# Performance work log

Measured on AMD Instinct MI355X. Metric: run time of the kernel, lower is better.

Reference implementation:

```python
import jax, jax.numpy as jnp
import numpy as np

S, B, D_MODEL, H = 2048, 2, 1024, 16
DH = D_MODEL // H
SCALE = 1.0 / np.sqrt(DH)
NEG_INF = jnp.float32(-1e30)


def setup_inputs() -> dict:
    key = jax.random.key(0)
    ks = jax.random.split(key, 12)
    std = 1.0 / np.sqrt(D_MODEL)
    inp = {
        "query": jax.random.normal(ks[0], (S, B, D_MODEL), jnp.float32),
        "key": jax.random.normal(ks[1], (S, B, D_MODEL), jnp.float32),
        "value": jax.random.normal(ks[2], (S, B, D_MODEL), jnp.float32),
        # causal mask, shape (seq_q, seq_k, 1) per prepare_mask asserts
        "mask": jnp.tril(jnp.ones((S, S), dtype=bool))[:, :, None],
        # params stored (in, out) for x @ W
        "Wq": jax.random.normal(ks[3], (D_MODEL, H * DH), jnp.float32) * std,
        "bq": jnp.zeros((H * DH,), jnp.float32),
        "Wk": jax.random.normal(ks[4], (D_MODEL, H * DH), jnp.float32) * std,
        "bk": jnp.zeros((H * DH,), jnp.float32),
        "Wv": jax.random.normal(ks[5], (D_MODEL, H * DH), jnp.float32) * std,
        "bv": jnp.zeros((H * DH,), jnp.float32),
        "Wo": jax.random.normal(ks[6], (D_MODEL, D_MODEL), jnp.float32) * std,
        "bo": jnp.zeros((D_MODEL,), jnp.float32),
    }
    return inp


def reference(query, key, value, mask, Wq, bq, Wk, bk, Wv, bv, Wo, bo):
    seq_len, batch, _ = query.shape
    # project and split heads: (S, B, H, DH)
    q = (query @ Wq + bq).reshape(seq_len, batch, H, DH)
    k = (key @ Wk + bk).reshape(key.shape[0], batch, H, DH)
    v = (value @ Wv + bv).reshape(value.shape[0], batch, H, DH)
    # scores: (seq_q, batch, heads, seq_k)
    scores = jnp.einsum("ibhd,jbhd->ibhj", q, k) * SCALE
    # mask (seq_q, seq_k, batch_or_1) -> broadcast to (seq_q, batch, 1, seq_k)
    m = jnp.transpose(mask, (0, 2, 1))[:, :, None, :]
    scores = jnp.where(m, scores, NEG_INF)
    attn = jax.nn.softmax(scores, axis=-1)  # dropout_prob=0.0 (eval)
    x = jnp.einsum("ibhj,jbhd->ibhd", attn, v)
    x = x.reshape(seq_len, batch, H * DH)
    return x @ Wo + bo
```

## Files before the change

### kernel.cpp

```cpp
#include <hip/hip_runtime.h>
#include <hip/hip_bf16.h>
#include <cstdint>

#define S_LEN 2048
#define BATCH 2
#define DM    1024
#define NH    16
#define DH    64
#define SL2E  0.18033688011112042f

typedef short s8v __attribute__((ext_vector_type(8)));
typedef float f4v __attribute__((ext_vector_type(4)));

__device__ __forceinline__ ushort f2bf(float x) {
  union { float f; uint32_t u; } v; v.f = x;
  uint32_t r = v.u + 0x7fffu + ((v.u >> 16) & 1u);
  return (ushort)(r >> 16);
}
__device__ __forceinline__ uint32_t fbits(float x) {
  union { float f; uint32_t u; } v; v.f = x; return v.u;
}
__device__ __forceinline__ uint32_t bfrnd(uint32_t u) {
  return u + 0x7fffu + ((u >> 16) & 1u);
}
__device__ __forceinline__ uint32_t packbf(uint32_t flo, uint32_t fhi) {
  return __builtin_amdgcn_perm(bfrnd(fhi), bfrnd(flo), 0x07060302u);
}

typedef __attribute__((address_space(1))) const void gas_void;
typedef __attribute__((address_space(3))) void las_void;
__device__ __forceinline__ void gld16(void* l, const void* g) {
  __builtin_amdgcn_global_load_lds((gas_void*)(uintptr_t)g,
                                   (las_void*)(uintptr_t)l, 16, 0, 0);
}

__global__ __launch_bounds__(256)
void wtrans(const float* W0, const float* W1, const float* W2, const float* W3,
            ushort* T0, ushort* T1, ushort* T2, ushort* T3) {
  const float* W; ushort* T;
  switch (blockIdx.z) {
    case 0:  W = W0; T = T0; break;
    case 1:  W = W1; T = T1; break;
    case 2:  W = W2; T = T2; break;
    default: W = W3; T = T3; break;
  }
  __shared__ ushort tile[32][33];
  const int n0 = blockIdx.x * 32, k0 = blockIdx.y * 32;
  const int tx = threadIdx.x, ty = threadIdx.y;
  #pragma unroll
  for (int r = ty; r < 32; r += 8)
    tile[r][tx] = f2bf(W[(size_t)(k0 + r) * DM + n0 + tx]);
  __syncthreads();
  #pragma unroll
  for (int r = ty; r < 32; r += 8)
    T[(size_t)(n0 + r) * DM + k0 + tx] = tile[tx][r];
}

__global__ __launch_bounds__(256)
void castx(const float* __restrict__ X0, const float* __restrict__ X1,
           const float* __restrict__ X2,
           ushort* __restrict__ O0, ushort* __restrict__ O1,
           ushort* __restrict__ O2) {
  const float* X; ushort* O;
  switch (blockIdx.y) {
    case 0:  X = X0; O = O0; break;
    case 1:  X = X1; O = O1; break;
    default: X = X2; O = O2; break;
  }
  const size_t i = ((size_t)blockIdx.x * 256 + threadIdx.x) * 4;
  const float4 v = *(const float4*)(X + i);
  ushort4 h;
  h.x = f2bf(v.x); h.y = f2bf(v.y); h.z = f2bf(v.z); h.w = f2bf(v.w);
  *(ushort4*)(O + i) = h;
}

__global__ __launch_bounds__(256)
void gemm_qkv(const ushort* __restrict__ Xq, const ushort* __restrict__ Xk,
              const ushort* __restrict__ Xv,
              const ushort* __restrict__ Wqt, const ushort* __restrict__ Wkt,
              const ushort* __restrict__ Wvt,
              const float* __restrict__ bq, const float* __restrict__ bk,
              const float* __restrict__ bv,
              ushort* __restrict__ Qh, ushort* __restrict__ Kh,
              ushort* __restrict__ Vt) {
  const int z = blockIdx.z;
  const ushort* A    = z == 0 ? Xq  : z == 1 ? Xk  : Xv;
  const ushort* Bt   = z == 0 ? Wqt : z == 1 ? Wkt : Wvt;
  const float*  bias = z == 0 ? bq  : z == 1 ? bk  : bv;

  __shared__ __align__(16) ushort lds[20480];
  ushort* ldsA = lds;
  ushort* ldsB = lds + 8192;

  const int tid = threadIdx.x, lane = tid & 63, w = tid >> 6;
  const int wr = w >> 1, wc = w & 1;
  const int lrow = lane & 15, quad = lane >> 4;
  const int m0 = blockIdx.x * 128, n0 = blockIdx.y * 128;

  const int srow = lane >> 3;
  const int scol = ((lane & 7) ^ srow) * 8;

  const ushort* gA[4]; ushort* lA[4];
  const ushort* gB[4]; ushort* lB[4];
  #pragma unroll
  for (int t = 0; t < 4; t++) {
    const int c = 4 * w + t;
    gA[t] = A  + (size_t)(m0 + c * 8 + srow) * DM + scol;
    lA[t] = &ldsA[c * 512];
    gB[t] = Bt + (size_t)(n0 + c * 8 + srow) * DM + scol;
    lB[t] = &ldsB[c * 512];
  }

  const int f8 = lrow & 7;
  const ushort *pa[2][4], *pb[2][4];
  #pragma unroll
  for (int kk = 0; kk < 2; kk++)
    #pragma unroll
    for (int i = 0; i < 4; i++) {
      pa[kk][i] = &ldsA[(wr * 64 + i * 16 + lrow) * 64 + (((kk * 4 + quad) ^ f8) * 8)];
      pb[kk][i] = &ldsB[(wc * 64 + i * 16 + lrow) * 64 + (((kk * 4 + quad) ^ f8) * 8)];
    }

  f4v acc[4][4];
  #pragma unroll
  for (int i = 0; i < 4; i++)
    #pragma unroll
    for (int j = 0; j < 4; j++)
      acc[i][j] = f4v{0.f, 0.f, 0.f, 0.f};

  for (int k0 = 0; k0 < DM; k0 += 64) {
    __syncthreads();
    #pragma unroll
    for (int t = 0; t < 4; t++) { gld16(lA[t], gA[t] + k0); gld16(lB[t], gB[t] + k0); }
    __syncthreads();
    #pragma unroll
    for (int kk = 0; kk < 2; kk++) {
      s8v af[4], bf[4];
      #pragma unroll
      for (int i = 0; i < 4; i++) af[i] = *(const s8v*)pa[kk][i];
      #pragma unroll
      for (int j = 0; j < 4; j++) bf[j] = *(const s8v*)pb[kk][j];
      #pragma unroll
      for (int i = 0; i < 4; i++)
        #pragma unroll
        for (int j = 0; j < 4; j++)
          acc[i][j] = __builtin_amdgcn_mfma_f32_16x16x32_bf16(af[i], bf[j], acc[i][j], 0, 0, 0);
    }
  }

  if (z <= 1) {
    ushort* O = (z == 0) ? Qh : Kh;
    #pragma unroll
    for (int i = 0; i < 4; i++)
      #pragma unroll
      for (int j = 0; j < 4; j++) {
        const int n = n0 + wc * 64 + j * 16 + lrow;
        const float bval = bias[n];
        const int mb = m0 + wr * 64 + i * 16 + quad * 4;
        #pragma unroll
        for (int r = 0; r < 4; r++) {
          const int m = mb + r;
          const int s = m >> 1, b = m & 1;
          const int h = n >> 6, d = n & 63;
          O[((size_t)(b * NH + h) * S_LEN + s) * DH + d] = f2bf(acc[i][j][r] + bval);
        }
      }
  } else {
    __syncthreads();
    ushort* tw = lds + w * 5120;
    #pragma unroll
    for (int i = 0; i < 4; i++)
      #pragma unroll
      for (int j = 0; j < 4; j++) {
        const int n_l = j * 16 + lrow;
        const float bval = bias[n0 + wc * 64 + n_l];
        const int sbase = i * 8 + quad * 2;
        const uint32_t p0 = packbf(fbits(acc[i][j][0] + bval), fbits(acc[i][j][2] + bval));
        const uint32_t p1 = packbf(fbits(acc[i][j][1] + bval), fbits(acc[i][j][3] + bval));
        *(uint32_t*)&tw[n_l * 40 + sbase]        = p0;
        *(uint32_t*)&tw[2560 + n_l * 40 + sbase] = p1;
      }
    const int s0 = (m0 >> 1) + wr * 32;
    #pragma unroll
    for (int b = 0; b < 2; b++)
      #pragma unroll
      for (int p = 0; p < 4; p++) {
        const int d_l = p * 16 + (lane >> 2);
        const int c   = lane & 3;
        const s8v v = *(const s8v*)&tw[b * 2560 + d_l * 40 + c * 8];
        const int n = n0 + wc * 64 + d_l;
        const int h = n >> 6, d = n & 63;
        *(s8v*)&Vt[((size_t)(b * NH + h) * DH + d) * S_LEN + s0 + c * 8] = v;
      }
  }
}

__global__ __launch_bounds__(256)
void attn(const ushort* __restrict__ Qh, const ushort* __restrict__ Kh,
          const ushort* __restrict__ Vt, ushort* __restrict__ X,
          float* __restrict__ Opart, float* __restrict__ lpart) {
  __shared__ __align__(16) ushort Klds[2 * 64 * 64];
  __shared__ __align__(16) ushort Vlds[2 * 64 * 64];
  __shared__ __align__(16) ushort Plds[4 * 32 * 72];

  const int tid = threadIdx.x, lane = tid & 63, w = tid >> 6;
  const int lrow = lane & 15, quad = lane >> 4;
  const int bh = blockIdx.x;
  const int slot = blockIdx.y;
  int qt, jlo, jhi, part;
  if (slot < 8) { qt = slot; jlo = 0; jhi = 2 * qt + 2; part = -1; }
  else {
    const int s2 = slot - 8;
    qt = 8 + (s2 >> 1);
    const int half = s2 & 1;
    jlo = half * (qt + 1);
    jhi = jlo + (qt + 1);
    part = s2;
  }
  const int iw = qt * 128 + w * 32;

  const int srow = lane >> 3;
  const int scol = ((lane & 7) ^ srow) * 8;
  const ushort* gK0 = Kh + ((size_t)bh * S_LEN + 2 * w * 8 + srow) * DH + scol;
  const ushort* gK1 = gK0 + 8 * DH;
  const ushort* gV0 = Vt + ((size_t)bh * DH + 2 * w * 8 + srow) * S_LEN + scol;
  const ushort* gV1 = gV0 + 8 * S_LEN;
  ushort* lK0 = &Klds[2 * w * 512]; ushort* lK1 = lK0 + 512;
  ushort* lV0 = &Vlds[2 * w * 512]; ushort* lV1 = lV0 + 512;

  s8v aq[2][2];
  #pragma unroll
  for (int is = 0; is < 2; is++)
    #pragma unroll
    for (int kk = 0; kk < 2; kk++)
      aq[is][kk] = *(const s8v*)(Qh + ((size_t)bh * S_LEN + iw + is * 16 + lrow) * DH +
                                 kk * 32 + quad * 8);

  const int f8 = lrow & 7;
  const ushort* pk[4][2]; const ushort* pv[4][2]; const ushort* pp[2][2];
  #pragma unroll
  for (int s4 = 0; s4 < 4; s4++)
    #pragma unroll
    for (int kk = 0; kk < 2; kk++) {
      pk[s4][kk] = &Klds[(s4 * 16 + lrow) * 64 + (((kk * 4 + quad) ^ f8) * 8)];
      pv[s4][kk] = &Vlds[(s4 * 16 + lrow) * 64 + (((kk * 4 + quad) ^ f8) * 8)];
    }
  #pragma unroll
  for (int is = 0; is < 2; is++)
    #pragma unroll
    for (int kk = 0; kk < 2; kk++)
      pp[is][kk] = &Plds[(w * 32 + is * 16 + lrow) * 72 + kk * 32 + quad * 8];
  ushort* pw = &Plds[w * 32 * 72];

  f4v o[2][4];
  float ls[2][4];
  #pragma unroll
  for (int is = 0; is < 2; is++) {
    #pragma unroll
    for (int d4 = 0; d4 < 4; d4++) o[is][d4] = f4v{0.f, 0.f, 0.f, 0.f};
    #pragma unroll
    for (int r = 0; r < 4; r++) ls[is][r] = 0.f;
  }

  {
    const int b0 = (jlo & 1) * 4096;
    const size_t j0 = (size_t)jlo * 64;
    gld16(lK0 + b0, gK0 + j0 * DH);
    gld16(lK1 + b0, gK1 + j0 * DH);
    gld16(lV0 + b0, gV0 + j0);
    gld16(lV1 + b0, gV1 + j0);
  }

  for (int jt = jlo; jt < jhi; jt++) {
    const int j0 = jt * 64;
    __syncthreads();
    const int cur = (jt & 1) * 4096;
    if (jt + 1 < jhi) {
      const int nxt = ((jt + 1) & 1) * 4096;
      const size_t jn = (size_t)(jt + 1) * 64;
      gld16(lK0 + nxt, gK0 + jn * DH);
      gld16(lK1 + nxt, gK1 + jn * DH);
      gld16(lV0 + nxt, gV0 + jn);
      gld16(lV1 + nxt, gV1 + jn);
    }
    if (j0 > iw + 31) continue;

    f4v sc[2][4];
    #pragma unroll
    for (int is = 0; is < 2; is++)
      #pragma unroll
      for (int s4 = 0; s4 < 4; s4++) sc[is][s4] = f4v{0.f, 0.f, 0.f, 0.f};
    #pragma unroll
    for (int s4 = 0; s4 < 4; s4++) {
      const s8v b0 = *(const s8v*)(pk[s4][0] + cur);
      const s8v b1 = *(const s8v*)(pk[s4][1] + cur);
      sc[0][s4] = __builtin_amdgcn_mfma_f32_16x16x32_bf16(aq[0][0], b0, sc[0][s4], 0, 0, 0);
      sc[1][s4] = __builtin_amdgcn_mfma_f32_16x16x32_bf16(aq[1][0], b0, sc[1][s4], 0, 0, 0);
      sc[0][s4] = __builtin_amdgcn_mfma_f32_16x16x32_bf16(aq[0][1], b1, sc[0][s4], 0, 0, 0);
      sc[1][s4] = __builtin_amdgcn_mfma_f32_16x16x32_bf16(aq[1][1], b1, sc[1][s4], 0, 0, 0);
    }

    const bool needmask = (j0 + 63) > iw;
    #pragma unroll
    for (int is = 0; is < 2; is++)
      #pragma unroll
      for (int s4 = 0; s4 < 4; s4++) {
        const int jg = j0 + s4 * 16 + lrow;
        #pragma unroll
        for (int r = 0; r < 4; r++) {
          float e = exp2f(sc[is][s4][r] * SL2E);
          if (needmask) {
            const int ig = iw + is * 16 + quad * 4 + r;
            e = (jg > ig) ? 0.f : e;
          }
          ls[is][r] += e;
          pw[(is * 16 + quad * 4 + r) * 72 + s4 * 16 + lrow] = f2bf(e);
        }
      }

    s8v ap[2][2];
    #pragma unroll
    for (int is = 0; is < 2; is++)
      #pragma unroll
      for (int kk = 0; kk < 2; kk++) ap[is][kk] = *(const s8v*)pp[is][kk];

    #pragma unroll
    for (int d4 = 0; d4 < 4; d4++) {
      const s8v v0 = *(const s8v*)(pv[d4][0] + cur);
      const s8v v1 = *(const s8v*)(pv[d4][1] + cur);
      o[0][d4] = __builtin_amdgcn_mfma_f32_16x16x32_bf16(ap[0][0], v0, o[0][d4], 0, 0, 0);
      o[1][d4] = __builtin_amdgcn_mfma_f32_16x16x32_bf16(ap[1][0], v0, o[1][d4], 0, 0, 0);
      o[0][d4] = __builtin_amdgcn_mfma_f32_16x16x32_bf16(ap[0][1], v1, o[0][d4], 0, 0, 0);
      o[1][d4] = __builtin_amdgcn_mfma_f32_16x16x32_bf16(ap[1][1], v1, o[1][d4], 0, 0, 0);
    }
  }

  #pragma unroll
  for (int msk = 1; msk < 16; msk <<= 1)
    #pragma unroll
    for (int is = 0; is < 2; is++)
      #pragma unroll
      for (int r = 0; r < 4; r++)
        ls[is][r] += __shfl_xor(ls[is][r], msk, 64);

  if (part < 0) {
    const int bb = bh >> 4, h = bh & 15;
    #pragma unroll
    for (int is = 0; is < 2; is++)
      #pragma unroll
      for (int r = 0; r < 4; r++) {
        const float inv = 1.0f / ls[is][r];
        const int ig = iw + is * 16 + quad * 4 + r;
        #pragma unroll
        for (int d4 = 0; d4 < 4; d4++)
          X[((size_t)ig * BATCH + bb) * DM + h * DH + d4 * 16 + lrow] =
              f2bf(o[is][d4][r] * inv);
      }
  } else {
    float* Op = Opart + ((size_t)(bh * 16 + part)) * 8192 + (size_t)w * 32 * 64;
    #pragma unroll
    for (int is = 0; is < 2; is++)
      #pragma unroll
      for (int r = 0; r < 4; r++) {
        const int row_l = is * 16 + quad * 4 + r;
        #pragma unroll
        for (int d4 = 0; d4 < 4; d4++)
          Op[row_l * 64 + d4 * 16 + lrow] = o[is][d4][r];
      }
    if (lrow == 0) {
      float* lp = lpart + (size_t)(bh * 16 + part) * 128 + w * 32;
      #pragma unroll
      for (int is = 0; is < 2; is++)
        #pragma unroll
        for (int r = 0; r < 4; r++)
          lp[is * 16 + quad * 4 + r] = ls[is][r];
    }
  }
}

__global__ __launch_bounds__(256)
void combine(const float* __restrict__ Opart, const float* __restrict__ lpart,
             ushort* __restrict__ X) {
  const size_t gid = (size_t)blockIdx.x * 256 + threadIdx.x;
  const int dv  = gid & 15;
  const int row = (gid >> 4) & 127;
  const int bh  = (gid >> 11) & 31;
  const int qt8 = gid >> 16;
  const int pa = qt8 * 2, pb = pa + 1;
  const size_t ba = ((size_t)(bh * 16 + pa)) * 8192 + row * 64 + dv * 4;
  const size_t bb_ = ((size_t)(bh * 16 + pb)) * 8192 + row * 64 + dv * 4;
  const float4 va = *(const float4*)(Opart + ba);
  const float4 vb = *(const float4*)(Opart + bb_);
  const float l = lpart[(size_t)(bh * 16 + pa) * 128 + row] +
                  lpart[(size_t)(bh * 16 + pb) * 128 + row];
  const float inv = 1.0f / l;
  const int qpos = (qt8 + 8) * 128 + row;
  const int b = bh >> 4, h = bh & 15;
  ushort4 hv;
  hv.x = f2bf((va.x + vb.x) * inv);
  hv.y = f2bf((va.y + vb.y) * inv);
  hv.z = f2bf((va.z + vb.z) * inv);
  hv.w = f2bf((va.w + vb.w) * inv);
  *(ushort4*)&X[(((size_t)qpos * BATCH + b) * NH + h) * DH + dv * 4] = hv;
}

__global__ __launch_bounds__(256)
void gemm_out(const ushort* __restrict__ A, const ushort* __restrict__ Bt,
              const float* __restrict__ bias, float* __restrict__ C) {
  __shared__ __align__(16) ushort ldsA[128 * 64];
  __shared__ __align__(16) ushort ldsB[128 * 64];

  const int tid = threadIdx.x, lane = tid & 63, w = tid >> 6;
  const int wr = w >> 1, wc = w & 1;
  const int lrow = lane & 15, quad = lane >> 4;
  const int m0 = blockIdx.x * 128, n0 = blockIdx.y * 128;

  const int srow = lane >> 3;
  const int scol = ((lane & 7) ^ srow) * 8;

  const ushort* gA[4]; ushort* lA[4];
  const ushort* gB[4]; ushort* lB[4];
  #pragma unroll
  for (int t = 0; t < 4; t++) {
    const int c = 4 * w + t;
    gA[t] = A  + (size_t)(m0 + c * 8 + srow) * DM + scol;
    lA[t] = &ldsA[c * 512];
    gB[t] = Bt + (size_t)(n0 + c * 8 + srow) * DM + scol;
    lB[t] = &ldsB[c * 512];
  }

  const int f8 = lrow & 7;
  const ushort *pa[2][4], *pb[2][4];
  #pragma unroll
  for (int kk = 0; kk < 2; kk++)
    #pragma unroll
    for (int i = 0; i < 4; i++) {
      pa[kk][i] = &ldsA[(wr * 64 + i * 16 + lrow) * 64 + (((kk * 4 + quad) ^ f8) * 8)];
      pb[kk][i] = &ldsB[(wc * 64 + i * 16 + lrow) * 64 + (((kk * 4 + quad) ^ f8) * 8)];
    }

  f4v acc[4][4];
  #pragma unroll
  for (int i = 0; i < 4; i++)
    #pragma unroll
    for (int j = 0; j < 4; j++)
      acc[i][j] = f4v{0.f, 0.f, 0.f, 0.f};

  for (int k0 = 0; k0 < DM; k0 += 64) {
    __syncthreads();
    #pragma unroll
    for (int t = 0; t < 4; t++) { gld16(lA[t], gA[t] + k0); gld16(lB[t], gB[t] + k0); }
    __syncthreads();
    #pragma unroll
    for (int kk = 0; kk < 2; kk++) {
      s8v af[4], bf[4];
      #pragma unroll
      for (int i = 0; i < 4; i++) af[i] = *(const s8v*)pa[kk][i];
      #pragma unroll
      for (int j = 0; j < 4; j++) bf[j] = *(const s8v*)pb[kk][j];
      #pragma unroll
      for (int i = 0; i < 4; i++)
        #pragma unroll
        for (int j = 0; j < 4; j++)
          acc[i][j] = __builtin_amdgcn_mfma_f32_16x16x32_bf16(af[i], bf[j], acc[i][j], 0, 0, 0);
    }
  }

  #pragma unroll
  for (int i = 0; i < 4; i++)
    #pragma unroll
    for (int j = 0; j < 4; j++) {
      const int n = n0 + wc * 64 + j * 16 + lrow;
      const float bval = bias[n];
      const int mb = m0 + wr * 64 + i * 16 + quad * 4;
      #pragma unroll
      for (int r = 0; r < 4; r++)
        C[(size_t)(mb + r) * DM + n] = acc[i][j][r] + bval;
    }
}

extern "C" void kernel_launch(void* const* d_in, const int* in_sizes, int n_in,
                              void* d_out, int out_size, void* d_ws, size_t ws_size,
                              hipStream_t stream) {
  const float* query = (const float*)d_in[0];
  const float* key_  = (const float*)d_in[1];
  const float* value = (const float*)d_in[2];
  const float* Wq = (const float*)d_in[4];
  const float* bq = (const float*)d_in[5];
  const float* Wk = (const float*)d_in[6];
  const float* bk = (const float*)d_in[7];
  const float* Wv = (const float*)d_in[8];
  const float* bv = (const float*)d_in[9];
  const float* Wo = (const float*)d_in[10];
  const float* bo = (const float*)d_in[11];

  ushort* Wqt = (ushort*)d_ws;
  ushort* Wkt = Wqt + (size_t)1024 * 1024;
  ushort* Wvt = Wkt + (size_t)1024 * 1024;
  ushort* Wot = Wvt + (size_t)1024 * 1024;
  ushort* Xbq = Wot + (size_t)1024 * 1024;
  ushort* Xbk = Xbq + (size_t)4 * 1024 * 1024;
  ushort* Xbv = Xbk + (size_t)4 * 1024 * 1024;
  ushort* Qh  = Xbv + (size_t)4 * 1024 * 1024;
  ushort* Kh  = Qh  + (size_t)4 * 1024 * 1024;
  ushort* Vt  = Kh  + (size_t)4 * 1024 * 1024;
  float*  Opart = (float*)Xbk;
  float*  lpart = (float*)(Vt + (size_t)4 * 1024 * 1024);
  ushort* Xa  = Xbq;

  wtrans<<<dim3(32, 32, 4), dim3(32, 8), 0, stream>>>(Wq, Wk, Wv, Wo,
                                                      Wqt, Wkt, Wvt, Wot);
  castx<<<dim3(4096, 3), 256, 0, stream>>>(query, key_, value, Xbq, Xbk, Xbv);
  gemm_qkv<<<dim3(32, 8, 3), 256, 0, stream>>>(Xbq, Xbk, Xbv,
                                               Wqt, Wkt, Wvt, bq, bk, bv,
                                               Qh, Kh, Vt);
  attn<<<dim3(32, 24), 256, 0, stream>>>(Qh, Kh, Vt, Xa, Opart, lpart);
  combine<<<2048, 256, 0, stream>>>(Opart, lpart, Xa);
  gemm_out<<<dim3(32, 8), 256, 0, stream>>>(Xa, Wot, bo, (float*)d_out);
}
```

Baseline: 262.0 us.

## Give each attention wave its own 32-row task and read K/V from global memory

Attention work is now split per wave instead of per block. Each wave takes one 32-row query strip, with the longest strips split in two and handled longest-first. K and V fragments are loaded straight from global memory into registers, which removes the shared-memory double buffer and the block-wide syncs. The QK MFMA operands are swapped so probabilities are written to LDS as packed 4-element bf16 stores. The weight-transpose and input-cast kernels are also merged into one launch. This trades LDS reuse of K/V across four waves for more global and L2 traffic, in exchange for finer load balancing and fewer syncs.

```diff
diff --git a/kernel.cpp b/kernel.cpp
--- a/kernel.cpp
+++ b/kernel.cpp
@@ -35,43 +35,34 @@
 }
 
 __global__ __launch_bounds__(256)
-void wtrans(const float* W0, const float* W1, const float* W2, const float* W3,
-            ushort* T0, ushort* T1, ushort* T2, ushort* T3) {
-  const float* W; ushort* T;
-  switch (blockIdx.z) {
-    case 0:  W = W0; T = T0; break;
-    case 1:  W = W1; T = T1; break;
-    case 2:  W = W2; T = T2; break;
-    default: W = W3; T = T3; break;
-  }
-  __shared__ ushort tile[32][33];
-  const int n0 = blockIdx.x * 32, k0 = blockIdx.y * 32;
-  const int tx = threadIdx.x, ty = threadIdx.y;
-  #pragma unroll
-  for (int r = ty; r < 32; r += 8)
-    tile[r][tx] = f2bf(W[(size_t)(k0 + r) * DM + n0 + tx]);
-  __syncthreads();
-  #pragma unroll
-  for (int r = ty; r < 32; r += 8)
-    T[(size_t)(n0 + r) * DM + k0 + tx] = tile[tx][r];
-}
-
-__global__ __launch_bounds__(256)
-void castx(const float* __restrict__ X0, const float* __restrict__ X1,
-           const float* __restrict__ X2,
-           ushort* __restrict__ O0, ushort* __restrict__ O1,
-           ushort* __restrict__ O2) {
-  const float* X; ushort* O;
-  switch (blockIdx.y) {
-    case 0:  X = X0; O = O0; break;
-    case 1:  X = X1; O = O1; break;
-    default: X = X2; O = O2; break;
-  }
-  const size_t i = ((size_t)blockIdx.x * 256 + threadIdx.x) * 4;
-  const float4 v = *(const float4*)(X + i);
-  ushort4 h;
-  h.x = f2bf(v.x); h.y = f2bf(v.y); h.z = f2bf(v.z); h.w = f2bf(v.w);
-  *(ushort4*)(O + i) = h;
+void prep(const float* W0, const float* W1, const float* W2, const float* W3,
+          ushort* T0, ushort* T1, ushort* T2, ushort* T3,
+          const float* X0, const float* X1, const float* X2,
+          ushort* O0, ushort* O1, ushort* O2) {
+  const int z = blockIdx.z;
+  if (z < 4) {
+    if (blockIdx.x >= 1024) return;
+    const float* W = z == 0 ? W0 : z == 1 ? W1 : z == 2 ? W2 : W3;
+    ushort*      T = z == 0 ? T0 : z == 1 ? T1 : z == 2 ? T2 : T3;
+    __shared__ ushort tile[32][33];
+    const int n0 = (blockIdx.x & 31) * 32, k0 = (blockIdx.x >> 5) * 32;
+    const int tx = threadIdx.x & 31, ty = threadIdx.x >> 5;
+    #pragma unroll
+    for (int r = ty; r < 32; r += 8)
+      tile[r][tx] = f2bf(W[(size_t)(k0 + r) * DM + n0 + tx]);
+    __syncthreads();
+    #pragma unroll
+    for (int r = ty; r < 32; r += 8)
+      T[(size_t)(n0 + r) * DM + k0 + tx] = tile[tx][r];
+  } else {
+    const float* X = z == 4 ? X0 : z == 5 ? X1 : X2;
+    ushort*      O = z == 4 ? O0 : z == 5 ? O1 : O2;
+    const size_t i = ((size_t)blockIdx.x * 256 + threadIdx.x) * 4;
+    const float4 v = *(const float4*)(X + i);
+    ushort4 h;
+    h.x = f2bf(v.x); h.y = f2bf(v.y); h.z = f2bf(v.z); h.w = f2bf(v.w);
+    *(ushort4*)(O + i) = h;
+  }
 }
 
 __global__ __launch_bounds__(256)
@@ -199,34 +190,31 @@
 void attn(const ushort* __restrict__ Qh, const ushort* __restrict__ Kh,
           const ushort* __restrict__ Vt, ushort* __restrict__ X,
           float* __restrict__ Opart, float* __restrict__ lpart) {
-  __shared__ __align__(16) ushort Klds[2 * 64 * 64];
-  __shared__ __align__(16) ushort Vlds[2 * 64 * 64];
-  __shared__ __align__(16) ushort Plds[4 * 32 * 72];
+  __shared__ __align__(16) ushort Plds[4][32 * 72];
 
   const int tid = threadIdx.x, lane = tid & 63, w = tid >> 6;
   const int lrow = lane & 15, quad = lane >> 4;
-  const int bh = blockIdx.x;
-  const int slot = blockIdx.y;
-  int qt, jlo, jhi, part;
-  if (slot < 8) { qt = slot; jlo = 0; jhi = 2 * qt + 2; part = -1; }
-  else {
-    const int s2 = slot - 8;
-    qt = 8 + (s2 >> 1);
-    const int half = s2 & 1;
-    jlo = half * (qt + 1);
-    jhi = jlo + (qt + 1);
-    part = s2;
-  }
-  const int iw = qt * 128 + w * 32;
-
-  const int srow = lane >> 3;
-  const int scol = ((lane & 7) ^ srow) * 8;
-  const ushort* gK0 = Kh + ((size_t)bh * S_LEN + 2 * w * 8 + srow) * DH + scol;
-  const ushort* gK1 = gK0 + 8 * DH;
-  const ushort* gV0 = Vt + ((size_t)bh * DH + 2 * w * 8 + srow) * S_LEN + scol;
-  const ushort* gV1 = gV0 + 8 * S_LEN;
-  ushort* lK0 = &Klds[2 * w * 512]; ushort* lK1 = lK0 + 512;
-  ushort* lV0 = &Vlds[2 * w * 512]; ushort* lV1 = lV0 + 512;
+
+  const int t = blockIdx.x * 4 + w;
+  int bh, r32, jlo, jhi, part;
+  if (t < 2048) {
+    bh = t & 31;
+    const int pid = t >> 5;
+    r32 = 63 - (pid >> 1);
+    const int nt = (r32 >> 1) + 1;
+    const int n1 = (nt + 1) >> 1;
+    const int half = pid & 1;
+    jlo = half ? n1 : 0;
+    jhi = half ? nt : n1;
+    part = pid;
+  } else {
+    const int u = t - 2048;
+    bh = u & 31;
+    r32 = 31 - (u >> 5);
+    jlo = 0; jhi = (r32 >> 1) + 1;
+    part = -1;
+  }
+  const int iw = r32 * 32;
 
   s8v aq[2][2];
   #pragma unroll
@@ -236,54 +224,31 @@
       aq[is][kk] = *(const s8v*)(Qh + ((size_t)bh * S_LEN + iw + is * 16 + lrow) * DH +
                                  kk * 32 + quad * 8);
 
-  const int f8 = lrow & 7;
-  const ushort* pk[4][2]; const ushort* pv[4][2]; const ushort* pp[2][2];
-  #pragma unroll
-  for (int s4 = 0; s4 < 4; s4++)
-    #pragma unroll
-    for (int kk = 0; kk < 2; kk++) {
-      pk[s4][kk] = &Klds[(s4 * 16 + lrow) * 64 + (((kk * 4 + quad) ^ f8) * 8)];
-      pv[s4][kk] = &Vlds[(s4 * 16 + lrow) * 64 + (((kk * 4 + quad) ^ f8) * 8)];
-    }
+  const ushort* Kb = Kh + ((size_t)bh * S_LEN + lrow) * DH + quad * 8;
+  const ushort* Vb = Vt + ((size_t)bh * DH + lrow) * S_LEN + quad * 8;
+  ushort* pwr = &Plds[w][lrow * 72];
+
+  f4v o[2][4];
+  float ls[2] = {0.f, 0.f};
   #pragma unroll
   for (int is = 0; is < 2; is++)
     #pragma unroll
-    for (int kk = 0; kk < 2; kk++)
-      pp[is][kk] = &Plds[(w * 32 + is * 16 + lrow) * 72 + kk * 32 + quad * 8];
-  ushort* pw = &Plds[w * 32 * 72];
-
-  f4v o[2][4];
-  float ls[2][4];
-  #pragma unroll
-  for (int is = 0; is < 2; is++) {
-    #pragma unroll
     for (int d4 = 0; d4 < 4; d4++) o[is][d4] = f4v{0.f, 0.f, 0.f, 0.f};
-    #pragma unroll
-    for (int r = 0; r < 4; r++) ls[is][r] = 0.f;
-  }
-
-  {
-    const int b0 = (jlo & 1) * 4096;
-    const size_t j0 = (size_t)jlo * 64;
-    gld16(lK0 + b0, gK0 + j0 * DH);
-    gld16(lK1 + b0, gK1 + j0 * DH);
-    gld16(lV0 + b0, gV0 + j0);
-    gld16(lV1 + b0, gV1 + j0);
-  }
 
   for (int jt = jlo; jt < jhi; jt++) {
     const int j0 = jt * 64;
-    __syncthreads();
-    const int cur = (jt & 1) * 4096;
-    if (jt + 1 < jhi) {
-      const int nxt = ((jt + 1) & 1) * 4096;
-      const size_t jn = (size_t)(jt + 1) * 64;
-      gld16(lK0 + nxt, gK0 + jn * DH);
-      gld16(lK1 + nxt, gK1 + jn * DH);
-      gld16(lV0 + nxt, gV0 + jn);
-      gld16(lV1 + nxt, gV1 + jn);
-    }
-    if (j0 > iw + 31) continue;
+    s8v kf[4][2];
+    #pragma unroll
+    for (int s4 = 0; s4 < 4; s4++)
+      #pragma unroll
+      for (int kk = 0; kk < 2; kk++)
+        kf[s4][kk] = *(const s8v*)(Kb + (size_t)(j0 + s4 * 16) * DH + kk * 32);
+    s8v vf[4][2];
+    #pragma unroll
+    for (int d4 = 0; d4 < 4; d4++)
+      #pragma unroll
+      for (int kt = 0; kt < 2; kt++)
+        vf[d4][kt] = *(const s8v*)(Vb + (size_t)(d4 * 16) * S_LEN + j0 + kt * 32);
 
     f4v sc[2][4];
     #pragma unroll
@@ -292,56 +257,57 @@
       for (int s4 = 0; s4 < 4; s4++) sc[is][s4] = f4v{0.f, 0.f, 0.f, 0.f};
     #pragma unroll
     for (int s4 = 0; s4 < 4; s4++) {
-      const s8v b0 = *(const s8v*)(pk[s4][0] + cur);
-      const s8v b1 = *(const s8v*)(pk[s4][1] + cur);
-      sc[0][s4] = __builtin_amdgcn_mfma_f32_16x16x32_bf16(aq[0][0], b0, sc[0][s4], 0, 0, 0);
-      sc[1][s4] = __builtin_amdgcn_mfma_f32_16x16x32_bf16(aq[1][0], b0, sc[1][s4], 0, 0, 0);
-      sc[0][s4] = __builtin_amdgcn_mfma_f32_16x16x32_bf16(aq[0][1], b1, sc[0][s4], 0, 0, 0);
-      sc[1][s4] = __builtin_amdgcn_mfma_f32_16x16x32_bf16(aq[1][1], b1, sc[1][s4], 0, 0, 0);
+      sc[0][s4] = __builtin_amdgcn_mfma_f32_16x16x32_bf16(kf[s4][0], aq[0][0], sc[0][s4], 0, 0, 0);
+      sc[1][s4] = __builtin_amdgcn_mfma_f32_16x16x32_bf16(kf[s4][0], aq[1][0], sc[1][s4], 0, 0, 0);
+      sc[0][s4] = __builtin_amdgcn_mfma_f32_16x16x32_bf16(kf[s4][1], aq[0][1], sc[0][s4], 0, 0, 0);
+      sc[1][s4] = __builtin_amdgcn_mfma_f32_16x16x32_bf16(kf[s4][1], aq[1][1], sc[1][s4], 0, 0, 0);
     }
 
     const bool needmask = (j0 + 63) > iw;
     #pragma unroll
+    for (int is = 0; is < 2; is++) {
+      const int ig = iw + is * 16 + lrow;
+      #pragma unroll
+      for (int s4 = 0; s4 < 4; s4++) {
+        float e0 = exp2f(sc[is][s4][0] * SL2E);
+        float e1 = exp2f(sc[is][s4][1] * SL2E);
+        float e2 = exp2f(sc[is][s4][2] * SL2E);
+        float e3 = exp2f(sc[is][s4][3] * SL2E);
+        if (needmask) {
+          const int jb = j0 + s4 * 16 + quad * 4;
+          e0 = (jb + 0 > ig) ? 0.f : e0;
+          e1 = (jb + 1 > ig) ? 0.f : e1;
+          e2 = (jb + 2 > ig) ? 0.f : e2;
+          e3 = (jb + 3 > ig) ? 0.f : e3;
+        }
+        ls[is] += (e0 + e1) + (e2 + e3);
+        uint2 pk2;
+        pk2.x = packbf(fbits(e0), fbits(e1));
+        pk2.y = packbf(fbits(e2), fbits(e3));
+        *(uint2*)&pwr[is * 16 * 72 + s4 * 16 + quad * 4] = pk2;
+      }
+    }
+
+    s8v ap[2][2];
+    #pragma unroll
     for (int is = 0; is < 2; is++)
       #pragma unroll
-      for (int s4 = 0; s4 < 4; s4++) {
-        const int jg = j0 + s4 * 16 + lrow;
-        #pragma unroll
-        for (int r = 0; r < 4; r++) {
-          float e = exp2f(sc[is][s4][r] * SL2E);
-          if (needmask) {
-            const int ig = iw + is * 16 + quad * 4 + r;
-            e = (jg > ig) ? 0.f : e;
-          }
-          ls[is][r] += e;
-          pw[(is * 16 + quad * 4 + r) * 72 + s4 * 16 + lrow] = f2bf(e);
-        }
-      }
-
-    s8v ap[2][2];
-    #pragma unroll
-    for (int is = 0; is < 2; is++)
-      #pragma unroll
-      for (int kk = 0; kk < 2; kk++) ap[is][kk] = *(const s8v*)pp[is][kk];
-
+      for (int kt = 0; kt < 2; kt++)
+        ap[is][kt] = *(const s8v*)&pwr[is * 16 * 72 + kt * 32 + quad * 8];
     #pragma unroll
     for (int d4 = 0; d4 < 4; d4++) {
-      const s8v v0 = *(const s8v*)(pv[d4][0] + cur);
-      const s8v v1 = *(const s8v*)(pv[d4][1] + cur);
-      o[0][d4] = __builtin_amdgcn_mfma_f32_16x16x32_bf16(ap[0][0], v0, o[0][d4], 0, 0, 0);
-      o[1][d4] = __builtin_amdgcn_mfma_f32_16x16x32_bf16(ap[1][0], v0, o[1][d4], 0, 0, 0);
-      o[0][d4] = __builtin_amdgcn_mfma_f32_16x16x32_bf16(ap[0][1], v1, o[0][d4], 0, 0, 0);
-      o[1][d4] = __builtin_amdgcn_mfma_f32_16x16x32_bf16(ap[1][1], v1, o[1][d4], 0, 0, 0);
-    }
-  }
-
-  #pragma unroll
-  for (int msk = 1; msk < 16; msk <<= 1)
-    #pragma unroll
-    for (int is = 0; is < 2; is++)
-      #pragma unroll
-      for (int r = 0; r < 4; r++)
-        ls[is][r] += __shfl_xor(ls[is][r], msk, 64);
+      o[0][d4] = __builtin_amdgcn_mfma_f32_16x16x32_bf16(ap[0][0], vf[d4][0], o[0][d4], 0, 0, 0);
+      o[1][d4] = __builtin_amdgcn_mfma_f32_16x16x32_bf16(ap[1][0], vf[d4][0], o[1][d4], 0, 0, 0);
+      o[0][d4] = __builtin_amdgcn_mfma_f32_16x16x32_bf16(ap[0][1], vf[d4][1], o[0][d4], 0, 0, 0);
+      o[1][d4] = __builtin_amdgcn_mfma_f32_16x16x32_bf16(ap[1][1], vf[d4][1], o[1][d4], 0, 0, 0);
+    }
+  }
+
+  #pragma unroll
+  for (int is = 0; is < 2; is++) {
+    ls[is] += __shfl_xor(ls[is], 16, 64);
+    ls[is] += __shfl_xor(ls[is], 32, 64);
+  }
 
   if (part < 0) {
     const int bb = bh >> 4, h = bh & 15;
@@ -349,15 +315,16 @@
     for (int is = 0; is < 2; is++)
       #pragma unroll
       for (int r = 0; r < 4; r++) {
-        const float inv = 1.0f / ls[is][r];
-        const int ig = iw + is * 16 + quad * 4 + r;
+        const float lv = __shfl(ls[is], quad * 16 + quad * 4 + r, 64);
+        const float inv = 1.0f / lv;
+        const int sg = iw + is * 16 + quad * 4 + r;
         #pragma unroll
         for (int d4 = 0; d4 < 4; d4++)
-          X[((size_t)ig * BATCH + bb) * DM + h * DH + d4 * 16 + lrow] =
+          X[((size_t)sg * BATCH + bb) * DM + h * DH + d4 * 16 + lrow] =
               f2bf(o[is][d4][r] * inv);
       }
   } else {
-    float* Op = Opart + ((size_t)(bh * 16 + part)) * 8192 + (size_t)w * 32 * 64;
+    float* Op = Opart + (size_t)(bh * 64 + part) * 2048;
     #pragma unroll
     for (int is = 0; is < 2; is++)
       #pragma unroll
@@ -367,13 +334,10 @@
         for (int d4 = 0; d4 < 4; d4++)
           Op[row_l * 64 + d4 * 16 + lrow] = o[is][d4][r];
       }
-    if (lrow == 0) {
-      float* lp = lpart + (size_t)(bh * 16 + part) * 128 + w * 32;
-      #pragma unroll
-      for (int is = 0; is < 2; is++)
-        #pragma unroll
-        for (int r = 0; r < 4; r++)
-          lp[is * 16 + quad * 4 + r] = ls[is][r];
+    if (quad == 0) {
+      float* lp = lpart + (size_t)(bh * 64 + part) * 32;
+      lp[lrow]      = ls[0];
+      lp[16 + lrow] = ls[1];
     }
   }
 }
@@ -382,26 +346,27 @@
 void combine(const float* __restrict__ Opart, const float* __restrict__ lpart,
              ushort* __restrict__ X) {
   const size_t gid = (size_t)blockIdx.x * 256 + threadIdx.x;
-  const int dv  = gid & 15;
-  const int row = (gid >> 4) & 127;
-  const int bh  = (gid >> 11) & 31;
-  const int qt8 = gid >> 16;
-  const int pa = qt8 * 2, pb = pa + 1;
-  const size_t ba = ((size_t)(bh * 16 + pa)) * 8192 + row * 64 + dv * 4;
-  const size_t bb_ = ((size_t)(bh * 16 + pb)) * 8192 + row * 64 + dv * 4;
+  const int dv    = gid & 15;
+  const int row_l = (gid >> 4) & 31;
+  const int k     = (gid >> 9) & 31;
+  const int bh    = gid >> 14;
+  const int r32 = 63 - k;
+  const int pa = 2 * k, pb = pa + 1;
+  const size_t ba = (size_t)(bh * 64 + pa) * 2048 + row_l * 64 + dv * 4;
+  const size_t bb_ = (size_t)(bh * 64 + pb) * 2048 + row_l * 64 + dv * 4;
   const float4 va = *(const float4*)(Opart + ba);
   const float4 vb = *(const float4*)(Opart + bb_);
-  const float l = lpart[(size_t)(bh * 16 + pa) * 128 + row] +
-                  lpart[(size_t)(bh * 16 + pb) * 128 + row];
+  const float l = lpart[(size_t)(bh * 64 + pa) * 32 + row_l] +
+                  lpart[(size_t)(bh * 64 + pb) * 32 + row_l];
   const float inv = 1.0f / l;
-  const int qpos = (qt8 + 8) * 128 + row;
+  const int sg = r32 * 32 + row_l;
   const int b = bh >> 4, h = bh & 15;
   ushort4 hv;
   hv.x = f2bf((va.x + vb.x) * inv);
   hv.y = f2bf((va.y + vb.y) * inv);
   hv.z = f2bf((va.z + vb.z) * inv);
   hv.w = f2bf((va.w + vb.w) * inv);
-  *(ushort4*)&X[(((size_t)qpos * BATCH + b) * NH + h) * DH + dv * 4] = hv;
+  *(ushort4*)&X[((size_t)sg * BATCH + b) * DM + h * DH + dv * 4] = hv;
 }
 
 __global__ __launch_bounds__(256)
@@ -508,13 +473,12 @@
   float*  lpart = (float*)(Vt + (size_t)4 * 1024 * 1024);
   ushort* Xa  = Xbq;
 
-  wtrans<<<dim3(32, 32, 4), dim3(32, 8), 0, stream>>>(Wq, Wk, Wv, Wo,
-                                                      Wqt, Wkt, Wvt, Wot);
-  castx<<<dim3(4096, 3), 256, 0, stream>>>(query, key_, value, Xbq, Xbk, Xbv);
+  prep<<<dim3(4096, 1, 7), 256, 0, stream>>>(Wq, Wk, Wv, Wo, Wqt, Wkt, Wvt, Wot,
+                                             query, key_, value, Xbq, Xbk, Xbv);
   gemm_qkv<<<dim3(32, 8, 3), 256, 0, stream>>>(Xbq, Xbk, Xbv,
                                                Wqt, Wkt, Wvt, bq, bk, bv,
                                                Qh, Kh, Vt);
-  attn<<<dim3(32, 24), 256, 0, stream>>>(Qh, Kh, Vt, Xa, Opart, lpart);
+  attn<<<768, 256, 0, stream>>>(Qh, Kh, Vt, Xa, Opart, lpart);
   combine<<<2048, 256, 0, stream>>>(Opart, lpart, Xa);
   gemm_out<<<dim3(32, 8), 256, 0, stream>>>(Xa, Wot, bo, (float*)d_out);
 }
```

Result: slower. 289.5 us (+10.5%).
